# Kernel optimization log

Hardware: AMD Instinct MI355X
Metric: run time of the kernel (lower is better)

## Reference

```python
import jax, jax.numpy as jnp
import numpy as np

B, S, D, H, E, F, K = 4, 1024, 1024, 16, 8, 4096, 2
HD = D // H  # 64
EPS = 1e-6


def _rmsnorm(x, w):
    return x * jax.lax.rsqrt(jnp.mean(x * x, axis=-1, keepdims=True) + EPS) * w


def _rope(x, cos, sin):
    # x: [B,S,H,HD]; cos/sin: [S,HD//2]
    b, s, h, hd = x.shape
    x2 = x.reshape(b, s, h, hd // 2, 2)
    xr, xi = x2[..., 0], x2[..., 1]
    c = cos[None, :, None, :]
    sn = sin[None, :, None, :]
    or_ = xr * c - xi * sn
    oi = xr * sn + xi * c
    return jnp.stack([or_, oi], axis=-1).reshape(b, s, h, hd)


def setup_inputs() -> dict:
    key = jax.random.key(0)
    ks = jax.random.split(key, 16)
    sc = 0.02
    # rotary tables (standard LLaMa rope)
    inv = 1.0 / (10000.0 ** (np.arange(0, HD, 2, dtype=np.float32) / HD))
    ang = np.outer(np.arange(S, dtype=np.float32), inv)
    return {
        "q": jax.random.normal(ks[0], (B, S, D), jnp.float32),
        "k": jax.random.normal(ks[1], (B, S, D), jnp.float32),
        "v": jax.random.normal(ks[2], (B, S, D), jnp.float32),
        "freqs_cos": jnp.asarray(np.cos(ang)),
        "freqs_sin": jnp.asarray(np.sin(ang)),
        "att_norm_w": jnp.ones((D,), jnp.float32),
        "ffn_norm_w": jnp.ones((D,), jnp.float32),
        "wq": jax.random.normal(ks[3], (D, D), jnp.float32) * sc,
        "wk": jax.random.normal(ks[4], (D, D), jnp.float32) * sc,
        "wv": jax.random.normal(ks[5], (D, D), jnp.float32) * sc,
        "wo": jax.random.normal(ks[6], (D, D), jnp.float32) * sc,
        "router_w": jax.random.normal(ks[7], (E, D), jnp.float32) * sc,
        "router_b": jnp.zeros((E,), jnp.float32),
        "w1": jax.random.normal(ks[8], (E, F, D), jnp.float32) * sc,
        "w2": jax.random.normal(ks[9], (E, D, F), jnp.float32) * sc,
        "w3": jax.random.normal(ks[10], (E, F, D), jnp.float32) * sc,
        "is_causal": 1,
    }


def _attention(qn, kn, vn, freqs_cos, freqs_sin, wq, wk, wv, wo, is_causal):
    b, s, d = qn.shape
    qh = (qn @ wq.T).reshape(b, s, H, HD)
    kh = (kn @ wk.T).reshape(b, s, H, HD)
    vh = (vn @ wv.T).reshape(b, s, H, HD)
    qh = _rope(qh, freqs_cos, freqs_sin)
    kh = _rope(kh, freqs_cos, freqs_sin)
    scores = jnp.einsum("bqhd,bkhd->bhqk", qh, kh) / jnp.sqrt(jnp.float32(HD))
    if is_causal:
        causal = jnp.tril(jnp.ones((s, s), bool))
        scores = jnp.where(causal[None, None], scores, jnp.float32(-1e30))
    probs = jax.nn.softmax(scores, axis=-1)
    out = jnp.einsum("bhqk,bkhd->bqhd", probs, vh).reshape(b, s, d)
    return out @ wo.T


def _sparse_moe(x, router_w, router_b, w1, w2, w3):
    # x: [B,S,D]
    flat = x.reshape(-1, x.shape[-1])  # [T,D]
    logits = flat @ router_w.T + router_b  # [T,E]
    top_v, top_i = jax.lax.top_k(logits, K)  # eval mode: no noise
    probs = jax.nn.softmax(top_v, axis=-1)  # softmax over -inf-filled == softmax over top-k
    gates = jnp.sum(jax.nn.one_hot(top_i, E, dtype=flat.dtype) * probs[..., None], axis=1)  # [T,E]
    y = jnp.zeros_like(flat)
    for e in range(E):  # fixed small expert loop; gate==0 for unselected tokens (faithful to masked dispatch)
        hgate = jax.nn.silu(flat @ w1[e].T) * (flat @ w3[e].T)  # SwiGLU FFN_LLaMa
        y = y + gates[:, e : e + 1] * (hgate @ w2[e].T)
    return y.reshape(x.shape)


def reference(q, k, v, freqs_cos, freqs_sin, att_norm_w, ffn_norm_w, wq, wk, wv, wo,
              router_w, router_b, w1, w2, w3, is_causal):
    qn = _rmsnorm(q, att_norm_w)
    # self-attention path: k = v = normed q (q.clone())
    h = q + _attention(qn, qn, qn, freqs_cos, freqs_sin, wq, wk, wv, wo, is_causal)
    out = h + _sparse_moe(_rmsnorm(h, ffn_norm_w), router_w, router_b, w1, w2, w3)
    return out
```

## Files before the change

kernel.cpp:

```cpp
#include <hip/hip_runtime.h>
#include <hip/hip_bf16.h>
#include <math.h>

#define NB 4
#define SQ 1024
#define DM 1024
#define NH 16
#define HDm 64
#define NE 8
#define FFd 4096
#define NTOK 4096
#define RTOT 10240
#define EPSF 1e-6f

typedef __attribute__((ext_vector_type(8))) short bf16x8_t;
typedef __attribute__((ext_vector_type(4))) float f32x4_t;
typedef const __attribute__((address_space(1))) void* gas_t;
typedef __attribute__((address_space(3))) void* las_t;

__device__ __forceinline__ float b2f(unsigned short u){
  return __uint_as_float(((unsigned int)u) << 16);
}
__device__ __forceinline__ unsigned short f2b(float f){
  __hip_bfloat16 h = __float2bfloat16(f);
  unsigned short u;
  __builtin_memcpy(&u, &h, 2);
  return u;
}

__global__ __launch_bounds__(256) void convert_k(const float* __restrict__ s,
                                                 unsigned short* __restrict__ d, int n4){
  int i = blockIdx.x*256 + threadIdx.x;
  if (i >= n4) return;
  float4 v = ((const float4*)s)[i];
  ushort4 o; o.x=f2b(v.x); o.y=f2b(v.y); o.z=f2b(v.z); o.w=f2b(v.w);
  ((ushort4*)d)[i] = o;
}

__global__ __launch_bounds__(256) void split_k(const float* __restrict__ s,
                                               unsigned short* __restrict__ hi,
                                               unsigned short* __restrict__ lo, int n4){
  int i = blockIdx.x*256 + threadIdx.x;
  if (i >= n4) return;
  float4 v = ((const float4*)s)[i];
  ushort4 h, l;
  h.x=f2b(v.x); l.x=f2b(v.x - b2f(h.x));
  h.y=f2b(v.y); l.y=f2b(v.y - b2f(h.y));
  h.z=f2b(v.z); l.z=f2b(v.z - b2f(h.z));
  h.w=f2b(v.w); l.w=f2b(v.w - b2f(h.w));
  ((ushort4*)hi)[i] = h;
  ((ushort4*)lo)[i] = l;
}

__global__ __launch_bounds__(256) void rmsnorm_k(const float* __restrict__ x,
                                                 const float* __restrict__ w,
                                                 float* __restrict__ o){
  int row = blockIdx.x; int t = threadIdx.x;
  float4 v = ((const float4*)(x + (size_t)row*DM))[t];
  float ss = v.x*v.x + v.y*v.y + v.z*v.z + v.w*v.w;
  #pragma unroll
  for (int d=32; d; d>>=1) ss += __shfl_down(ss, d, 64);
  __shared__ float red[4];
  int wid = t>>6, ln = t&63;
  if (ln==0) red[wid] = ss;
  __syncthreads();
  float tot = red[0]+red[1]+red[2]+red[3];
  float sc = 1.0f/sqrtf(tot*(1.0f/DM) + EPSF);
  float4 wv = ((const float4*)w)[t];
  float4 ov = { v.x*sc*wv.x, v.y*sc*wv.y, v.z*sc*wv.z, v.w*sc*wv.w };
  ((float4*)(o + (size_t)row*DM))[t] = ov;
}

__global__ __launch_bounds__(256) void rmsnorm_split_k(const float* __restrict__ x,
                                                       const float* __restrict__ w,
                                                       unsigned short* __restrict__ hi,
                                                       unsigned short* __restrict__ lo){
  int row = blockIdx.x; int t = threadIdx.x;
  float4 v = ((const float4*)(x + (size_t)row*DM))[t];
  float ss = v.x*v.x + v.y*v.y + v.z*v.z + v.w*v.w;
  #pragma unroll
  for (int d=32; d; d>>=1) ss += __shfl_down(ss, d, 64);
  __shared__ float red[4];
  int wid = t>>6, ln = t&63;
  if (ln==0) red[wid] = ss;
  __syncthreads();
  float tot = red[0]+red[1]+red[2]+red[3];
  float sc = 1.0f/sqrtf(tot*(1.0f/DM) + EPSF);
  float4 wv = ((const float4*)w)[t];
  float4 ov = { v.x*sc*wv.x, v.y*sc*wv.y, v.z*sc*wv.z, v.w*sc*wv.w };
  ushort4 h, l;
  h.x=f2b(ov.x); l.x=f2b(ov.x - b2f(h.x));
  h.y=f2b(ov.y); l.y=f2b(ov.y - b2f(h.y));
  h.z=f2b(ov.z); l.z=f2b(ov.z - b2f(h.z));
  h.w=f2b(ov.w); l.w=f2b(ov.w - b2f(h.w));
  ((ushort4*)(hi + (size_t)row*DM))[t] = h;
  ((ushort4*)(lo + (size_t)row*DM))[t] = l;
}

__global__ __launch_bounds__(256) void gemm_nt_split(
  const unsigned short* __restrict__ Ah, const unsigned short* __restrict__ Al,
  const unsigned short* __restrict__ Bh0, const unsigned short* __restrict__ Bl0,
  const unsigned short* __restrict__ Bh1, const unsigned short* __restrict__ Bl1,
  const unsigned short* __restrict__ Bh2, const unsigned short* __restrict__ Bl2,
  float* __restrict__ C0, float* __restrict__ C1, float* __restrict__ C2,
  const float* __restrict__ resid, int Kd, int Ncols)
{
  const unsigned short* Bh = (blockIdx.z==0)?Bh0:(blockIdx.z==1)?Bh1:Bh2;
  const unsigned short* Bl = (blockIdx.z==0)?Bl0:(blockIdx.z==1)?Bl1:Bl2;
  float* C = (blockIdx.z==0)?C0:(blockIdx.z==1)?C1:C2;
  __shared__ unsigned short AsH[128*32];
  __shared__ unsigned short AsL[128*32];
  __shared__ unsigned short BsH[128*32];
  __shared__ unsigned short BsL[128*32];
  const int t = threadIdx.x;
  const int w = t>>6, lane = t&63;
  const int wm = w>>1, wn = w&1;
  const int lm = lane&15, fk = (lane>>4)*8;
  const int row0 = blockIdx.y*128, col0 = blockIdx.x*128;
  f32x4_t acc[4][4];
  #pragma unroll
  for (int i=0;i<4;i++)
    #pragma unroll
    for (int j=0;j<4;j++){ f32x4_t z = {0.f,0.f,0.f,0.f}; acc[i][j]=z; }
  for (int k0=0;k0<Kd;k0+=32){
    __syncthreads();
    #pragma unroll
    for (int j=0;j<2;j++){
      const int chunk = j*4 + w;
      const int gt = chunk*64 + lane;
      const int rw_ = gt>>2, kp = (gt&3)*8;
      const size_t aoff = (size_t)(row0+rw_)*Kd + k0 + kp;
      const size_t boff = (size_t)(col0+rw_)*Kd + k0 + kp;
      __builtin_amdgcn_global_load_lds((gas_t)(Ah + aoff), (las_t)(AsH + chunk*512), 16, 0, 0);
      __builtin_amdgcn_global_load_lds((gas_t)(Al + aoff), (las_t)(AsL + chunk*512), 16, 0, 0);
      __builtin_amdgcn_global_load_lds((gas_t)(Bh + boff), (las_t)(BsH + chunk*512), 16, 0, 0);
      __builtin_amdgcn_global_load_lds((gas_t)(Bl + boff), (las_t)(BsL + chunk*512), 16, 0, 0);
    }
    __syncthreads();
    bf16x8_t ah[4], al[4], bh[4], bl[4];
    #pragma unroll
    for (int f=0;f<4;f++){
      const size_t ao = (size_t)(wm*64 + f*16 + lm)*32 + fk;
      const size_t bo = (size_t)(wn*64 + f*16 + lm)*32 + fk;
      ah[f] = *(const bf16x8_t*)(AsH + ao);
      al[f] = *(const bf16x8_t*)(AsL + ao);
      bh[f] = *(const bf16x8_t*)(BsH + bo);
      bl[f] = *(const bf16x8_t*)(BsL + bo);
    }
    #pragma unroll
    for (int i=0;i<4;i++)
      #pragma unroll
      for (int j=0;j<4;j++){
        acc[i][j] = __builtin_amdgcn_mfma_f32_16x16x32_bf16(ah[i], bh[j], acc[i][j], 0, 0, 0);
        acc[i][j] = __builtin_amdgcn_mfma_f32_16x16x32_bf16(al[i], bh[j], acc[i][j], 0, 0, 0);
        acc[i][j] = __builtin_amdgcn_mfma_f32_16x16x32_bf16(ah[i], bl[j], acc[i][j], 0, 0, 0);
      }
  }
  const int rbase = row0 + wm*64 + (lane>>4)*4;
  const int cbase = col0 + wn*64 + lm;
  #pragma unroll
  for (int i=0;i<4;i++)
    #pragma unroll
    for (int j=0;j<4;j++)
      #pragma unroll
      for (int r=0;r<4;r++){
        const size_t idx = (size_t)(rbase + i*16 + r)*Ncols + cbase + j*16;
        float v = acc[i][j][r];
        if (resid) v += resid[idx];
        C[idx] = v;
      }
}

__global__ __launch_bounds__(256) void rope_bf16_k(const float* __restrict__ qh,
  const float* __restrict__ kh, const float* __restrict__ fc, const float* __restrict__ fs,
  unsigned short* __restrict__ qb, unsigned short* __restrict__ kb){
  int idx = blockIdx.x*256 + threadIdx.x;
  if (idx >= NTOK*NH*32) return;
  int i = idx & 31;
  int h = (idx>>5) & (NH-1);
  int n = idx >> 9;
  int s = n & (SQ-1);
  float c = fc[s*32+i], sn = fs[s*32+i];
  size_t base = (size_t)n*DM + h*HDm + 2*i;
  float xr = qh[base], xi = qh[base+1];
  float or_ = (xr*c - xi*sn) * 0.125f;
  float oi  = (xr*sn + xi*c) * 0.125f;
  unsigned int pq = (unsigned int)f2b(or_) | ((unsigned int)f2b(oi) << 16);
  *(unsigned int*)(qb + base) = pq;
  xr = kh[base]; xi = kh[base+1];
  or_ = xr*c - xi*sn; oi = xr*sn + xi*c;
  unsigned int pk = (unsigned int)f2b(or_) | ((unsigned int)f2b(oi) << 16);
  *(unsigned int*)(kb + base) = pk;
}

__global__ __launch_bounds__(256) void vtrans_k(const float* __restrict__ vh,
                                                unsigned short* __restrict__ vT){
  __shared__ unsigned short Lt[64][72];
  const int st = blockIdx.x, bh = blockIdx.y;
  const int b = bh >> 4, h = bh & 15;
  const int t = threadIdx.x;
  const int s0 = st*64;
  const int sr = t >> 2, hq = (t & 3) * 16;
  const float* src = vh + ((size_t)(b*SQ + s0 + sr))*DM + h*HDm + hq;
  #pragma unroll
  for (int i=0;i<4;i++){
    float4 v = *(const float4*)(src + 4*i);
    Lt[hq+4*i+0][sr] = f2b(v.x);
    Lt[hq+4*i+1][sr] = f2b(v.y);
    Lt[hq+4*i+2][sr] = f2b(v.z);
    Lt[hq+4*i+3][sr] = f2b(v.w);
  }
  __syncthreads();
  const int hd = t >> 2, sq = (t & 3) * 16;
  unsigned short* dst = vT + ((size_t)bh*HDm + hd)*SQ + s0 + sq;
  #pragma unroll
  for (int i=0;i<2;i++){
    bf16x8_t x = *(const bf16x8_t*)&Lt[hd][sq + 8*i];
    *(bf16x8_t*)(dst + 8*i) = x;
  }
}

__global__ __launch_bounds__(256) void flash_mfma_k(
  const unsigned short* __restrict__ qb, const unsigned short* __restrict__ kb,
  const unsigned short* __restrict__ vT,
  unsigned short* __restrict__ ctxh, unsigned short* __restrict__ ctxl,
  const int* __restrict__ causp)
{
  __shared__ unsigned short Qs[2*64*32];
  __shared__ unsigned short Ks[2*64*32];
  __shared__ unsigned short Vt[2*64*32];
  __shared__ unsigned short Ps[2*64*32];
  const int qt = blockIdx.x;
  const int bh = blockIdx.y;
  const int b = bh >> 4, h = bh & 15;
  const int t = threadIdx.x;
  const int w = t >> 6, lane = t & 63;
  const int lm = lane & 15, g = lane >> 4, fk = g * 8;
  const int q0 = qt * 64;
  const size_t qkoff = (size_t)b * SQ * DM + (size_t)h * HDm;
  const size_t voff  = ((size_t)bh * HDm) * SQ;

  #pragma unroll
  for (int j=0;j<2;j++){
    const int s = j*4 + w;
    const int c = s >> 2, r0 = (s & 3) * 16;
    const int row = r0 + (lane >> 2), kp = (lane & 3) * 8;
    __builtin_amdgcn_global_load_lds((gas_t)(qb + qkoff + (size_t)(q0+row)*DM + c*32 + kp),
                                     (las_t)(Qs + s*512), 16, 0, 0);
  }
  __syncthreads();
  bf16x8_t aq0 = *(const bf16x8_t*)(Qs + 0*2048 + (w*16+lm)*32 + fk);
  bf16x8_t aq1 = *(const bf16x8_t*)(Qs + 1*2048 + (w*16+lm)*32 + fk);

  const int causal = *causp;
  const int ktmax = causal ? qt : (SQ/64 - 1);
  f32x4_t O[4];
  #pragma unroll
  for (int j=0;j<4;j++){ f32x4_t z={0.f,0.f,0.f,0.f}; O[j]=z; }
  float mrow[4], lrow[4];
  #pragma unroll
  for (int r=0;r<4;r++){ mrow[r] = -3e30f; lrow[r] = 0.f; }

  for (int kt=0; kt<=ktmax; ++kt){
    const int k0 = kt*64;
    __syncthreads();
    #pragma unroll
    for (int j=0;j<2;j++){
      const int s = j*4 + w;
      const int c = s >> 2, r0 = (s & 3) * 16;
      const int row = r0 + (lane >> 2), kp = (lane & 3) * 8;
      __builtin_amdgcn_global_load_lds((gas_t)(kb + qkoff + (size_t)(k0+row)*DM + c*32 + kp),
                                       (las_t)(Ks + s*512), 16, 0, 0);
      __builtin_amdgcn_global_load_lds((gas_t)(vT + voff + (size_t)row*SQ + k0 + c*32 + kp),
                                       (las_t)(Vt + s*512), 16, 0, 0);
    }
    __syncthreads();

    f32x4_t Sv[4];
    #pragma unroll
    for (int j=0;j<4;j++){ f32x4_t z={0.f,0.f,0.f,0.f}; Sv[j]=z; }
    #pragma unroll
    for (int j=0;j<4;j++){
      bf16x8_t b0 = *(const bf16x8_t*)(Ks + 0*2048 + (j*16+lm)*32 + fk);
      bf16x8_t b1 = *(const bf16x8_t*)(Ks + 1*2048 + (j*16+lm)*32 + fk);
      Sv[j] = __builtin_amdgcn_mfma_f32_16x16x32_bf16(aq0, b0, Sv[j], 0, 0, 0);
      Sv[j] = __builtin_amdgcn_mfma_f32_16x16x32_bf16(aq1, b1, Sv[j], 0, 0, 0);
    }
    const int rowq = q0 + w*16 + g*4;
    if (causal && kt == qt){
      #pragma unroll
      for (int j=0;j<4;j++){
        const int col = k0 + j*16 + lm;
        #pragma unroll
        for (int r=0;r<4;r++)
          if (col > rowq + r) Sv[j][r] = -3e30f;
      }
    }
    float alpha[4];
    #pragma unroll
    for (int r=0;r<4;r++){
      float m_ = fmaxf(fmaxf(Sv[0][r],Sv[1][r]), fmaxf(Sv[2][r],Sv[3][r]));
      #pragma unroll
      for (int d=1; d<16; d<<=1) m_ = fmaxf(m_, __shfl_xor(m_, d, 64));
      const float mn = fmaxf(mrow[r], m_);
      alpha[r] = __expf(mrow[r] - mn);
      mrow[r] = mn;
    }
    #pragma unroll
    for (int r=0;r<4;r++){
      const int qrow = w*16 + g*4 + r;
      float rs = 0.f;
      #pragma unroll
      for (int j=0;j<4;j++){
        const float p = __expf(Sv[j][r] - mrow[r]);
        rs += p;
        const int key5 = (((j&1)<<4) | lm) ^ (g<<3);
        Ps[(j>>1)*2048 + qrow*32 + key5] = f2b(p);
      }
      #pragma unroll
      for (int d=1; d<16; d<<=1) rs += __shfl_xor(rs, d, 64);
      lrow[r] = lrow[r]*alpha[r] + rs;
      #pragma unroll
      for (int j=0;j<4;j++) O[j][r] *= alpha[r];
    }
    const int fkp = fk ^ (((lm>>2)&3)<<3);
    bf16x8_t pa0 = *(const bf16x8_t*)(Ps + 0*2048 + (w*16+lm)*32 + fkp);
    bf16x8_t pa1 = *(const bf16x8_t*)(Ps + 1*2048 + (w*16+lm)*32 + fkp);
    #pragma unroll
    for (int j=0;j<4;j++){
      bf16x8_t v0 = *(const bf16x8_t*)(Vt + 0*2048 + (j*16+lm)*32 + fk);
      bf16x8_t v1 = *(const bf16x8_t*)(Vt + 1*2048 + (j*16+lm)*32 + fk);
      O[j] = __builtin_amdgcn_mfma_f32_16x16x32_bf16(pa0, v0, O[j], 0, 0, 0);
      O[j] = __builtin_amdgcn_mfma_f32_16x16x32_bf16(pa1, v1, O[j], 0, 0, 0);
    }
  }
  #pragma unroll
  for (int r=0;r<4;r++){
    const float il = 1.0f / lrow[r];
    const size_t rowtok = (size_t)(q0 + w*16 + g*4 + r);
    #pragma unroll
    for (int j=0;j<4;j++){
      const float v = O[j][r] * il;
      const unsigned short hi = f2b(v);
      const float lo = v - b2f(hi);
      const size_t idx = qkoff + rowtok*DM + j*16 + lm;
      ctxh[idx] = hi;
      ctxl[idx] = f2b(lo);
    }
  }
}

__global__ __launch_bounds__(256) void router_k(
  const float* __restrict__ hn, const float* __restrict__ rw, const float* __restrict__ rb,
  int* __restrict__ topi, float* __restrict__ topp, int* __restrict__ counts)
{
  const int n = blockIdx.x, t = threadIdx.x;
  float4 x = ((const float4*)(hn + (size_t)n*DM))[t];
  float p[NE];
  #pragma unroll
  for (int e=0;e<NE;e++){
    float4 wv = ((const float4*)(rw + (size_t)e*DM))[t];
    p[e] = x.x*wv.x + x.y*wv.y + x.z*wv.z + x.w*wv.w;
  }
  #pragma unroll
  for (int e=0;e<NE;e++)
    #pragma unroll
    for (int d=32; d; d>>=1) p[e] += __shfl_down(p[e], d, 64);
  __shared__ float red[4][NE];
  int wid=t>>6, ln=t&63;
  if (ln==0){
    #pragma unroll
    for (int e=0;e<NE;e++) red[wid][e]=p[e];
  }
  __syncthreads();
  if (t==0){
    float v1=-3e30f, v2=-3e30f; int i1=0, i2=0;
    for (int e=0;e<NE;e++){
      float v = red[0][e]+red[1][e]+red[2][e]+red[3][e]+rb[e];
      if (v > v1){ v2=v1;i2=i1; v1=v;i1=e; }
      else if (v > v2){ v2=v;i2=e; }
    }
    float ex = expf(v2-v1);
    float g1 = 1.0f/(1.0f+ex);
    float g2 = ex*g1;
    topi[2*n]=i1; topi[2*n+1]=i2;
    topp[2*n]=g1; topp[2*n+1]=g2;
    atomicAdd(&counts[i1],1); atomicAdd(&counts[i2],1);
  }
}

__global__ void offsets_k(const int* __restrict__ counts, int* __restrict__ offs){
  if (blockIdx.x==0 && threadIdx.x==0){
    int run=0;
    for (int e=0;e<NE;e++){ offs[e]=run; run += (counts[e]+255)&~255; }
    offs[NE]=run;
  }
}

__global__ __launch_bounds__(256) void assign_k(const int* __restrict__ topi,
  const int* __restrict__ offs, int* __restrict__ cursor,
  int* __restrict__ list, int* __restrict__ inv){
  int t = blockIdx.x*256 + threadIdx.x;
  if (t >= NTOK*2) return;
  int e = topi[t];
  int slot = atomicAdd(&cursor[e], 1);
  int pos = offs[e] + slot;
  list[pos] = t>>1;
  inv[t] = pos;
}

__global__ __launch_bounds__(256) void gather_k(const float* __restrict__ hn,
  const int* __restrict__ offs, const int* __restrict__ counts, const int* __restrict__ list,
  unsigned short* __restrict__ xg){
  const int p = blockIdx.x;
  if (p >= offs[NE]) return;
  int e=0;
  while (offs[e+1] <= p) ++e;
  const int t = threadIdx.x;
  ushort4 o;
  if (p - offs[e] < counts[e]){
    int n = list[p];
    float4 x = ((const float4*)(hn + (size_t)n*DM))[t];
    o.x=f2b(x.x); o.y=f2b(x.y); o.z=f2b(x.z); o.w=f2b(x.w);
  } else { o.x=0; o.y=0; o.z=0; o.w=0; }
  ((ushort4*)(xg + (size_t)p*DM))[t] = o;
}

__global__ __launch_bounds__(512, 2) void gemm_moe_bf16(
  const unsigned short* __restrict__ Aall, const unsigned short* __restrict__ Wall,
  unsigned short* __restrict__ Call, const int* __restrict__ offs, int Kd, int Ncols)
{
  __shared__ unsigned short As[2*256*64];
  __shared__ unsigned short Bs[2*256*64];
  const int Gx = gridDim.x;
  const int nwg = Gx * gridDim.y;
  const int orig = blockIdx.y * Gx + blockIdx.x;
  const int wg = (orig & 7) * (nwg >> 3) + (orig >> 3);
  const int ry = wg / Gx, cx = wg - ry*Gx;
  const int row0 = ry * 256;
  if (row0 >= offs[NE]) return;
  int e = 0;
  while (offs[e+1] <= row0) ++e;
  const unsigned short* Wp = Wall + (size_t)e * Ncols * Kd;
  const int col0 = cx * 256;

  const int t = threadIdx.x;
  const int w = t >> 6, lane = t & 63;
  const int wm = w >> 2, wn = w & 3;
  const int lm = lane & 15, g = lane >> 4;
  const int lsub = lane >> 3;
  const int scol = (((lane & 7) ^ lsub) << 3);
  const int swzr = (lm & 7) << 4;

  f32x4_t acc[8][4];
  #pragma unroll
  for (int i=0;i<8;i++)
    #pragma unroll
    for (int j=0;j<4;j++){ f32x4_t z={0.f,0.f,0.f,0.f}; acc[i][j]=z; }

  const int KT = Kd >> 6;
  auto stage = [&](int buf, int k0){
    #pragma unroll
    for (int j=0;j<4;j++){
      const int s = j*8 + w;
      const int rl = s*8 + lsub;
      __builtin_amdgcn_global_load_lds(
        (gas_t)(Aall + (size_t)(row0+rl)*Kd + k0 + scol),
        (las_t)(As + buf*16384 + s*512), 16, 0, 0);
      __builtin_amdgcn_global_load_lds(
        (gas_t)(Wp + (size_t)(col0+rl)*Kd + k0 + scol),
        (las_t)(Bs + buf*16384 + s*512), 16, 0, 0);
    }
  };

  stage(0, 0);
  __syncthreads();
  int cur = 0;
  for (int kt=0; kt<KT; ++kt){
    if (kt+1 < KT) stage(cur^1, (kt+1)<<6);
    const unsigned short* Ab = As + cur*16384;
    const unsigned short* Bb = Bs + cur*16384;
    #pragma unroll
    for (int half=0; half<2; ++half){
      const int cb = (half<<6) | (g<<4);
      const int co = (cb ^ swzr) >> 1;
      bf16x8_t a[8], bfr[4];
      #pragma unroll
      for (int f=0;f<8;f++)
        a[f] = *(const bf16x8_t*)(Ab + (wm*128 + f*16 + lm)*64 + co);
      #pragma unroll
      for (int j=0;j<4;j++)
        bfr[j] = *(const bf16x8_t*)(Bb + (wn*64 + j*16 + lm)*64 + co);
      __builtin_amdgcn_s_setprio(1);
      #pragma unroll
      for (int i=0;i<8;i++)
        #pragma unroll
        for (int j=0;j<4;j++)
          acc[i][j] = __builtin_amdgcn_mfma_f32_16x16x32_bf16(a[i], bfr[j], acc[i][j], 0, 0, 0);
      __builtin_amdgcn_s_setprio(0);
    }
    __syncthreads();
    cur ^= 1;
  }

  #pragma unroll
  for (int i=0;i<8;i++){
    const int grow = row0 + wm*128 + i*16 + g*4;
    #pragma unroll
    for (int j=0;j<4;j++){
      const int gcol = col0 + wn*64 + j*16 + lm;
      #pragma unroll
      for (int r=0;r<4;r++)
        Call[(size_t)(grow + r)*Ncols + gcol] = f2b(acc[i][j][r]);
    }
  }
}

__global__ __launch_bounds__(256) void silu_mul_k(unsigned short* __restrict__ h1,
                                                  const unsigned short* __restrict__ h3){
  size_t i = (size_t)blockIdx.x*256 + threadIdx.x;
  ushort4 a = ((const ushort4*)h1)[i];
  ushort4 b = ((const ushort4*)h3)[i];
  ushort4 o;
  float fa, fb, s_;
  fa=b2f(a.x); fb=b2f(b.x); s_=fa/(1.f+__expf(-fa)); o.x=f2b(s_*fb);
  fa=b2f(a.y); fb=b2f(b.y); s_=fa/(1.f+__expf(-fa)); o.y=f2b(s_*fb);
  fa=b2f(a.z); fb=b2f(b.z); s_=fa/(1.f+__expf(-fa)); o.z=f2b(s_*fb);
  fa=b2f(a.w); fb=b2f(b.w); s_=fa/(1.f+__expf(-fa)); o.w=f2b(s_*fb);
  ((ushort4*)h1)[i] = o;
}

__global__ __launch_bounds__(256) void combine_k(const float* __restrict__ h,
  const unsigned short* __restrict__ yb, const float* __restrict__ topp,
  const int* __restrict__ inv, float* __restrict__ out)
{
  const int n = blockIdx.x, t = threadIdx.x;
  const int p0 = inv[2*n], p1 = inv[2*n+1];
  const float g0 = topp[2*n], g1 = topp[2*n+1];
  float4 hv = ((const float4*)(h + (size_t)n*DM))[t];
  ushort4 y0 = ((const ushort4*)(yb + (size_t)p0*DM))[t];
  ushort4 y1 = ((const ushort4*)(yb + (size_t)p1*DM))[t];
  float4 ov;
  ov.x = hv.x + g0*b2f(y0.x) + g1*b2f(y1.x);
  ov.y = hv.y + g0*b2f(y0.y) + g1*b2f(y1.y);
  ov.z = hv.z + g0*b2f(y0.z) + g1*b2f(y1.z);
  ov.w = hv.w + g0*b2f(y0.w) + g1*b2f(y1.w);
  ((float4*)(out + (size_t)n*DM))[t] = ov;
}

extern "C" void kernel_launch(void* const* d_in, const int* in_sizes, int n_in,
                              void* d_out, int out_size, void* d_ws, size_t ws_size,
                              hipStream_t stream)
{
  (void)in_sizes; (void)n_in; (void)out_size; (void)ws_size;
  const float* q    = (const float*)d_in[0];
  const float* fc   = (const float*)d_in[3];
  const float* fs   = (const float*)d_in[4];
  const float* attw = (const float*)d_in[5];
  const float* ffnw = (const float*)d_in[6];
  const float* wq   = (const float*)d_in[7];
  const float* wk   = (const float*)d_in[8];
  const float* wv   = (const float*)d_in[9];
  const float* wo   = (const float*)d_in[10];
  const float* rw   = (const float*)d_in[11];
  const float* rb   = (const float*)d_in[12];
  const float* w1   = (const float*)d_in[13];
  const float* w2   = (const float*)d_in[14];
  const float* w3   = (const float*)d_in[15];
  const int*   caus = (const int*)d_in[16];
  float* out = (float*)d_out;

  char* ws = (char*)d_ws;
  size_t off = 0;
  auto take = [&](size_t bytes)->char*{ char* r = ws + off; off += (bytes + 255) & ~(size_t)255; return r; };
  unsigned short* qnh = (unsigned short*)take((size_t)NTOK*DM*2);
  unsigned short* qnl = (unsigned short*)take((size_t)NTOK*DM*2);
  float* qh   = (float*)take((size_t)NTOK*DM*4);
  float* kh   = (float*)take((size_t)NTOK*DM*4);
  float* vh   = (float*)take((size_t)NTOK*DM*4);
  float* hbuf = (float*)take((size_t)NTOK*DM*4);
  unsigned short* h1  = (unsigned short*)take((size_t)RTOT*FFd*2);
  unsigned short* h3  = (unsigned short*)take((size_t)RTOT*FFd*2);
  unsigned short* yb  = (unsigned short*)take((size_t)RTOT*DM*2);
  unsigned short* w1b = (unsigned short*)take((size_t)NE*FFd*DM*2);
  unsigned short* w3b = (unsigned short*)take((size_t)NE*FFd*DM*2);
  unsigned short* w2b = (unsigned short*)take((size_t)NE*FFd*DM*2);
  int*   counts = (int*)take(64);
  int*   cursor = counts + 8;
  int*   offs   = (int*)take(64);
  int*   topi   = (int*)take((size_t)NTOK*2*4);
  float* topp   = (float*)take((size_t)NTOK*2*4);
  int*   list   = (int*)take((size_t)RTOT*4);
  int*   inv    = (int*)take((size_t)NTOK*2*4);

  unsigned short* ctxh = qnh;
  unsigned short* ctxl = qnl;
  float* hn = kh;
  unsigned short* xg = yb;
  unsigned short* wqh = (unsigned short*)h1;
  unsigned short* wql = wqh + (size_t)DM*DM;
  unsigned short* wkh = wql + (size_t)DM*DM;
  unsigned short* wkl = wkh + (size_t)DM*DM;
  unsigned short* wvh = wkl + (size_t)DM*DM;
  unsigned short* wvl = wvh + (size_t)DM*DM;
  unsigned short* woh = wvl + (size_t)DM*DM;
  unsigned short* wol = woh + (size_t)DM*DM;
  unsigned short* qb  = wqh + 8*(size_t)DM*DM;
  unsigned short* kb  = qb + (size_t)NTOK*DM;
  unsigned short* vTb = (unsigned short*)h3;

  const int nw4 = NE*FFd*DM/4;
  convert_k<<<nw4/256, 256, 0, stream>>>(w1, w1b, nw4);
  convert_k<<<nw4/256, 256, 0, stream>>>(w3, w3b, nw4);
  convert_k<<<nw4/256, 256, 0, stream>>>(w2, w2b, nw4);

  const int nwq4 = DM*DM/4;
  split_k<<<nwq4/256, 256, 0, stream>>>(wq, wqh, wql, nwq4);
  split_k<<<nwq4/256, 256, 0, stream>>>(wk, wkh, wkl, nwq4);
  split_k<<<nwq4/256, 256, 0, stream>>>(wv, wvh, wvl, nwq4);
  split_k<<<nwq4/256, 256, 0, stream>>>(wo, woh, wol, nwq4);

  rmsnorm_split_k<<<NTOK, 256, 0, stream>>>(q, attw, qnh, qnl);
  gemm_nt_split<<<dim3(8,32,3), 256, 0, stream>>>(qnh, qnl,
      wqh, wql, wkh, wkl, wvh, wvl, qh, kh, vh, nullptr, DM, DM);
  rope_bf16_k<<<NTOK*NH*32/256, 256, 0, stream>>>(qh, kh, fc, fs, qb, kb);
  vtrans_k<<<dim3(SQ/64, NB*NH), 256, 0, stream>>>(vh, vTb);
  flash_mfma_k<<<dim3(SQ/64, NB*NH), 256, 0, stream>>>(qb, kb, vTb, ctxh, ctxl, caus);
  gemm_nt_split<<<dim3(8,32,1), 256, 0, stream>>>(ctxh, ctxl,
      woh, wol, woh, wol, woh, wol, hbuf, hbuf, hbuf, q, DM, DM);
  rmsnorm_k<<<NTOK, 256, 0, stream>>>(hbuf, ffnw, hn);

  hipMemsetAsync(counts, 0, 64, stream);
  router_k<<<NTOK, 256, 0, stream>>>(hn, rw, rb, topi, topp, counts);
  offsets_k<<<1, 64, 0, stream>>>(counts, offs);
  assign_k<<<NTOK*2/256, 256, 0, stream>>>(topi, offs, cursor, list, inv);
  gather_k<<<RTOT, 256, 0, stream>>>(hn, offs, counts, list, xg);

  gemm_moe_bf16<<<dim3(FFd/256, RTOT/256), 512, 0, stream>>>(xg, w1b, h1, offs, DM, FFd);
  gemm_moe_bf16<<<dim3(FFd/256, RTOT/256), 512, 0, stream>>>(xg, w3b, h3, offs, DM, FFd);
  silu_mul_k<<<RTOT*FFd/4/256, 256, 0, stream>>>(h1, h3);
  gemm_moe_bf16<<<dim3(DM/256, RTOT/256), 512, 0, stream>>>(h1, w2b, yb, offs, FFd, DM);
  combine_k<<<NTOK, 256, 0, stream>>>(hbuf, yb, topp, inv, out);
}
```

Measured before the change: 1.216 ms.

## Merge w1/w3 MoE GEMMs into one launch and restructure LDS pipeline with explicit barriers

The two expert up-projection GEMMs (w1 and w3) now run as a single launch, with the column index choosing which weight and output buffer each workgroup uses. Inside the GEMM, the trailing __syncthreads is replaced by an explicit vmcnt wait plus raw s_barrier. The LDS-fragment loads and MFMA bursts are split into four interleaved phases separated by barriers, so all waves move in lockstep. The intent is to remove one launch tail, overlap the next tile's prefetch with compute, and cut register pressure from holding eight A fragments at once. The extra barriers per k-step could add stalls.

Result: slower. 1.271 ms (+4.5%).

```diff
diff --git a/kernel.cpp b/kernel.cpp
--- a/kernel.cpp
+++ b/kernel.cpp
@@ -27,6 +27,10 @@
   __builtin_memcpy(&u, &h, 2);
   return u;
 }
+
+#define PBAR() do{ __builtin_amdgcn_sched_barrier(0); \
+                   asm volatile("s_barrier" ::: "memory"); \
+                   __builtin_amdgcn_sched_barrier(0); }while(0)
 
 __global__ __launch_bounds__(256) void convert_k(const float* __restrict__ s,
                                                  unsigned short* __restrict__ d, int n4){
@@ -427,8 +431,10 @@
 }
 
 __global__ __launch_bounds__(512, 2) void gemm_moe_bf16(
-  const unsigned short* __restrict__ Aall, const unsigned short* __restrict__ Wall,
-  unsigned short* __restrict__ Call, const int* __restrict__ offs, int Kd, int Ncols)
+  const unsigned short* __restrict__ Aall,
+  const unsigned short* __restrict__ W0c, const unsigned short* __restrict__ W1c,
+  unsigned short* __restrict__ C0c, unsigned short* __restrict__ C1c,
+  const int* __restrict__ offs, int Kd, int Ncols, int xsplit)
 {
   __shared__ unsigned short As[2*256*64];
   __shared__ unsigned short Bs[2*256*64];
@@ -441,8 +447,10 @@
   if (row0 >= offs[NE]) return;
   int e = 0;
   while (offs[e+1] <= row0) ++e;
-  const unsigned short* Wp = Wall + (size_t)e * Ncols * Kd;
-  const int col0 = cx * 256;
+  const int sel = cx / xsplit;
+  const unsigned short* Wp = (sel ? W1c : W0c) + (size_t)e * Ncols * Kd;
+  unsigned short* Cp = sel ? C1c : C0c;
+  const int col0 = (cx - sel*xsplit) * 256;
 
   const int t = threadIdx.x;
   const int w = t >> 6, lane = t & 63;
@@ -474,32 +482,68 @@
   };
 
   stage(0, 0);
-  __syncthreads();
   int cur = 0;
   for (int kt=0; kt<KT; ++kt){
-    if (kt+1 < KT) stage(cur^1, (kt+1)<<6);
+    if (kt+1 < KT){
+      stage(cur^1, (kt+1)<<6);
+      asm volatile("s_waitcnt vmcnt(8)" ::: "memory");
+    } else {
+      asm volatile("s_waitcnt vmcnt(0)" ::: "memory");
+    }
+    PBAR();
     const unsigned short* Ab = As + cur*16384;
     const unsigned short* Bb = Bs + cur*16384;
-    #pragma unroll
-    for (int half=0; half<2; ++half){
-      const int cb = (half<<6) | (g<<4);
-      const int co = (cb ^ swzr) >> 1;
-      bf16x8_t a[8], bfr[4];
-      #pragma unroll
-      for (int f=0;f<8;f++)
-        a[f] = *(const bf16x8_t*)(Ab + (wm*128 + f*16 + lm)*64 + co);
+    const int co0 = (((0<<6) | (g<<4)) ^ swzr) >> 1;
+    const int co1 = (((1<<6) | (g<<4)) ^ swzr) >> 1;
+    bf16x8_t a[8], bfr[4];
+    #pragma unroll
+    for (int f=0;f<4;f++) a[f]   = *(const bf16x8_t*)(Ab + (wm*128 + f*16 + lm)*64 + co0);
+    #pragma unroll
+    for (int j=0;j<4;j++) bfr[j] = *(const bf16x8_t*)(Bb + (wn*64  + j*16 + lm)*64 + co0);
+    PBAR();
+    __builtin_amdgcn_s_setprio(1);
+    #pragma unroll
+    for (int i=0;i<4;i++)
       #pragma unroll
       for (int j=0;j<4;j++)
-        bfr[j] = *(const bf16x8_t*)(Bb + (wn*64 + j*16 + lm)*64 + co);
-      __builtin_amdgcn_s_setprio(1);
-      #pragma unroll
-      for (int i=0;i<8;i++)
-        #pragma unroll
-        for (int j=0;j<4;j++)
-          acc[i][j] = __builtin_amdgcn_mfma_f32_16x16x32_bf16(a[i], bfr[j], acc[i][j], 0, 0, 0);
-      __builtin_amdgcn_s_setprio(0);
-    }
-    __syncthreads();
+        acc[i][j] = __builtin_amdgcn_mfma_f32_16x16x32_bf16(a[i], bfr[j], acc[i][j], 0, 0, 0);
+    __builtin_amdgcn_s_setprio(0);
+    PBAR();
+    #pragma unroll
+    for (int f=0;f<4;f++) a[4+f] = *(const bf16x8_t*)(Ab + (wm*128 + (4+f)*16 + lm)*64 + co0);
+    PBAR();
+    __builtin_amdgcn_s_setprio(1);
+    #pragma unroll
+    for (int i=4;i<8;i++)
+      #pragma unroll
+      for (int j=0;j<4;j++)
+        acc[i][j] = __builtin_amdgcn_mfma_f32_16x16x32_bf16(a[i], bfr[j], acc[i][j], 0, 0, 0);
+    __builtin_amdgcn_s_setprio(0);
+    PBAR();
+    #pragma unroll
+    for (int f=0;f<4;f++) a[f]   = *(const bf16x8_t*)(Ab + (wm*128 + f*16 + lm)*64 + co1);
+    #pragma unroll
+    for (int j=0;j<4;j++) bfr[j] = *(const bf16x8_t*)(Bb + (wn*64  + j*16 + lm)*64 + co1);
+    PBAR();
+    __builtin_amdgcn_s_setprio(1);
+    #pragma unroll
+    for (int i=0;i<4;i++)
+      #pragma unroll
+      for (int j=0;j<4;j++)
+        acc[i][j] = __builtin_amdgcn_mfma_f32_16x16x32_bf16(a[i], bfr[j], acc[i][j], 0, 0, 0);
+    __builtin_amdgcn_s_setprio(0);
+    PBAR();
+    #pragma unroll
+    for (int f=0;f<4;f++) a[4+f] = *(const bf16x8_t*)(Ab + (wm*128 + (4+f)*16 + lm)*64 + co1);
+    PBAR();
+    __builtin_amdgcn_s_setprio(1);
+    #pragma unroll
+    for (int i=4;i<8;i++)
+      #pragma unroll
+      for (int j=0;j<4;j++)
+        acc[i][j] = __builtin_amdgcn_mfma_f32_16x16x32_bf16(a[i], bfr[j], acc[i][j], 0, 0, 0);
+    __builtin_amdgcn_s_setprio(0);
+    PBAR();
     cur ^= 1;
   }
 
@@ -511,7 +555,7 @@
       const int gcol = col0 + wn*64 + j*16 + lm;
       #pragma unroll
       for (int r=0;r<4;r++)
-        Call[(size_t)(grow + r)*Ncols + gcol] = f2b(acc[i][j][r]);
+        Cp[(size_t)(grow + r)*Ncols + gcol] = f2b(acc[i][j][r]);
     }
   }
 }
@@ -636,9 +680,8 @@
   assign_k<<<NTOK*2/256, 256, 0, stream>>>(topi, offs, cursor, list, inv);
   gather_k<<<RTOT, 256, 0, stream>>>(hn, offs, counts, list, xg);
 
-  gemm_moe_bf16<<<dim3(FFd/256, RTOT/256), 512, 0, stream>>>(xg, w1b, h1, offs, DM, FFd);
-  gemm_moe_bf16<<<dim3(FFd/256, RTOT/256), 512, 0, stream>>>(xg, w3b, h3, offs, DM, FFd);
+  gemm_moe_bf16<<<dim3(32, RTOT/256), 512, 0, stream>>>(xg, w1b, w3b, h1, h3, offs, DM, FFd, 16);
   silu_mul_k<<<RTOT*FFd/4/256, 256, 0, stream>>>(h1, h3);
-  gemm_moe_bf16<<<dim3(DM/256, RTOT/256), 512, 0, stream>>>(h1, w2b, yb, offs, FFd, DM);
+  gemm_moe_bf16<<<dim3(4, RTOT/256), 512, 0, stream>>>(h1, w2b, w2b, yb, yb, offs, FFd, DM, 4);
   combine_k<<<NTOK, 256, 0, stream>>>(hbuf, yb, topp, inv, out);
 }
```
